# Kernel tuning notes

Hardware: AMD Instinct MI355X
Metric: run time of the kernel (lower is better)

## Reference

```python
import jax, jax.numpy as jnp
import numpy as np

H = 16; W = 16; C_IN = 32; RNN_IN = 64; HID = 128; OUT = 512; B = 512


def _upsample_bilinear_ac(x, oh, ow):
    """Bilinear upsample with align_corners=True (matches nn.UpsamplingBilinear2d). x: (B,C,h,w)."""
    h, w = x.shape[2], x.shape[3]
    ys = (jnp.arange(oh, dtype=jnp.float32) * (h - 1) / (oh - 1))
    y0 = jnp.floor(ys).astype(jnp.int32)
    y1 = jnp.minimum(y0 + 1, h - 1)
    wy = (ys - y0.astype(jnp.float32))[None, None, :, None]
    xs = (jnp.arange(ow, dtype=jnp.float32) * (w - 1) / (ow - 1))
    x0 = jnp.floor(xs).astype(jnp.int32)
    x1 = jnp.minimum(x0 + 1, w - 1)
    wx = (xs - x0.astype(jnp.float32))[None, None, None, :]
    rows = x[:, :, y0, :] * (1.0 - wy) + x[:, :, y1, :] * wy  # (B,C,oh,w)
    out = rows[:, :, :, x0] * (1.0 - wx) + rows[:, :, :, x1] * wx  # (B,C,oh,ow)
    return out


def setup_inputs() -> dict:
    key = jax.random.key(0)
    ks = jax.random.split(key, 8)
    def winit(k, shape, fan_in):
        return jax.random.normal(k, shape, jnp.float32) / np.float32(np.sqrt(fan_in))
    return {
        "x": jax.random.normal(ks[0], (B, C_IN, H, W), jnp.float32),
        "h0": jax.random.normal(ks[1], (B, HID), jnp.float32),
        "W_in": winit(ks[2], (RNN_IN, C_IN), C_IN),
        "b_in": jnp.zeros((RNN_IN,), jnp.float32),
        "W_ih": winit(ks[3], (HID, RNN_IN), RNN_IN),
        "b_ih": jnp.zeros((HID,), jnp.float32),
        "W_hh": winit(ks[4], (HID, HID), HID),
        "b_hh": jnp.zeros((HID,), jnp.float32),
        "W_out": winit(ks[5], (OUT, HID), HID),
        "b_out": jnp.zeros((OUT,), jnp.float32),
    }


def reference(x, h0, W_in, b_in, W_ih, b_ih, W_hh, b_hh, W_out, b_out):
    b = x.shape[0]
    # (B,C,H,W) -> (B,L,C), L = H*W raster order
    x_seq = x.transpose(0, 2, 3, 1).reshape(b, H * W, C_IN)
    proj = x_seq @ W_in.T + b_in                      # (B,L,RNN_IN)
    pre = proj @ W_ih.T + b_ih                        # (B,L,HID), input part of RNNCell precomputed

    def step(h, p_t):
        h_new = jnp.tanh(p_t + h @ W_hh.T + b_hh)
        return h_new, h_new

    _, hs = jax.lax.scan(step, h0, pre.transpose(1, 0, 2))  # (L,B,HID)
    hs_map = hs.reshape(H, W, b, HID).transpose(2, 3, 0, 1)  # (B,HID,H,W)
    up = _upsample_bilinear_ac(hs_map, 2 * H, 2 * W)         # (B,HID,32,32)
    act = up * jnp.clip(up + 3.0, 0.0, 6.0) * (1.0 / 6.0)    # hardswish
    pooled = act.mean(axis=(2, 3))                           # (B,HID)
    return pooled @ W_out.T + b_out
```

## Files before the change

### kernel.cpp

```cpp
#include <hip/hip_runtime.h>

#define L 256
#define BATCH 512
#define CIN 32
#define HIDN 128
#define OUTN 512

typedef _Float16 f16x8 __attribute__((ext_vector_type(8)));
typedef float f32x4 __attribute__((ext_vector_type(4)));

#define MFMA16(a, b, c) __builtin_amdgcn_mfma_f32_16x16x32_f16(a, b, c, 0, 0, 0)

static __device__ __forceinline__ unsigned short f16b(_Float16 h) {
    unsigned short u; __builtin_memcpy(&u, &h, 2); return u;
}


__global__ __launch_bounds__(512, 1) void rnn_kernel(
    const float* __restrict__ x, const float* __restrict__ h0,
    const float* __restrict__ W_in, const float* __restrict__ b_in,
    const float* __restrict__ W_ih, const float* __restrict__ b_ih,
    const float* __restrict__ W_hh, const float* __restrict__ b_hh,
    unsigned short* __restrict__ hs)
{
    const int tid = threadIdx.x;
    const int bb = blockIdx.x;
    const int lane = tid & 63;
    const int w = tid >> 6;
    const int n = lane & 15;
    const int q = lane >> 4;

    __shared__ unsigned short hbuf[2][16][HIDN];
    __shared__ unsigned short xcl[2][16][64][8];
    __shared__ float wih_s[128][65];
    __shared__ float win_s[64][32];
    __shared__ float bin_s[64];

    float4 xr[4];
    auto issue_chunk = [&](int ci) {
#pragma unroll
        for (int r = 0; r < 4; ++r) {
            int i = tid + r * 512;
            int nn = i >> 7, cc = (i >> 2) & 31, tq = i & 3;
            xr[r] = *(const float4*)(x + (((size_t)bb * 16 + nn) * CIN + cc) * L + ci * 16 + tq * 4);
        }
    };
    auto write_chunk = [&](int buf) {
#pragma unroll
        for (int r = 0; r < 4; ++r) {
            int i = tid + r * 512;
            int nn = i >> 7, cc = (i >> 2) & 31, tq = i & 3;
            int gr = ((cc >> 3) * 16 + (nn ^ ((cc >> 3) << 2))) ^ tq;
            float vv[4] = {xr[r].x, xr[r].y, xr[r].z, xr[r].w};
#pragma unroll
            for (int k = 0; k < 4; ++k)
                xcl[buf][tq * 4 + k][gr][cc & 7] = f16b((_Float16)vv[k]);
        }
    };

    issue_chunk(0);

    for (int i = tid; i < 128 * 64; i += 512) wih_s[i >> 6][i & 63] = W_ih[i];
    for (int i = tid; i < 64 * 32; i += 512) ((float*)win_s)[i] = W_in[i];
    if (tid < 64) bin_s[tid] = b_in[tid];

    if (tid < 256) {
        const int ni = tid >> 4, gi = tid & 15;
        const float4* src = (const float4*)(h0 + ((size_t)bb * 16 + ni) * HIDN + gi * 8);
        float4 a = src[0], b4 = src[1];
        float vv[8] = {a.x, a.y, a.z, a.w, b4.x, b4.y, b4.z, b4.w};
        unsigned short o[8];
#pragma unroll
        for (int i = 0; i < 8; ++i) o[i] = f16b((_Float16)vv[i]);
        *(uint4*)&hbuf[0][ni][(gi ^ (ni & 7)) * 8] = *(uint4*)o;
    }
    __syncthreads();

    const int jr = w * 16 + n;
    f16x8 Ah[4], Al[4];
    const float* wrow = W_hh + jr * HIDN;
#pragma unroll
    for (int kc = 0; kc < 4; ++kc) {
        float4 v0 = *(const float4*)(wrow + kc * 32 + q * 8);
        float4 v1 = *(const float4*)(wrow + kc * 32 + q * 8 + 4);
        float vv[8] = {v0.x, v0.y, v0.z, v0.w, v1.x, v1.y, v1.z, v1.w};
        f16x8 H, Lo;
#pragma unroll
        for (int i = 0; i < 8; ++i) {
            _Float16 hi = (_Float16)vv[i];
            H[i] = hi;
            Lo[i] = (_Float16)(vv[i] - (float)hi);
        }
        Ah[kc] = H; Al[kc] = Lo;
    }
    float acc8[8];
#pragma unroll
    for (int i = 0; i < 8; ++i) acc8[i] = 0.f;
    for (int m = 0; m < 64; ++m) {
        float wv = wih_s[jr][m];
        const float* wc = &win_s[m][q * 8];
#pragma unroll
        for (int i = 0; i < 8; ++i) acc8[i] += wv * wc[i];
    }
    f16x8 Axh, Axl;
#pragma unroll
    for (int i = 0; i < 8; ++i) {
        _Float16 hi = (_Float16)acc8[i];
        Axh[i] = hi;
        Axl[i] = (_Float16)(acc8[i] - (float)hi);
    }
    const int jb0 = w * 16 + q * 4;
    float bs4[4];
#pragma unroll
    for (int r = 0; r < 4; ++r) bs4[r] = b_ih[jb0 + r] + b_hh[jb0 + r];
    for (int m = 0; m < 64; ++m) {
        float bm = bin_s[m];
#pragma unroll
        for (int r = 0; r < 4; ++r) bs4[r] += wih_s[jb0 + r][m] * bm;
    }
    f32x4 bp = (f32x4){bs4[0], bs4[1], bs4[2], bs4[3]};
    const f32x4 zero4 = (f32x4){0.f, 0.f, 0.f, 0.f};

    write_chunk(0);
    issue_chunk(1);
    __syncthreads();

    unsigned short* hsp = hs + ((size_t)bb * 16 + n) * HIDN + w * 16 + q * 4;
    const int G = (w * 2 + (q >> 1)) ^ (n & 7);
    const int sw = n & 7;
    const int grs = q * 16 + (n ^ (q << 2));

    f16x8 xb0, xb1;
    xb0 = *(const f16x8*)&xcl[0][0][grs][0];

#define STEP(T, IN, OUT, OFF, XCUR, XNEXT)                                     \
    {                                                                          \
        f16x8 Bh0 = *(const f16x8*)&hbuf[IN][n][((0 + q) ^ sw) * 8];           \
        f16x8 Bh1 = *(const f16x8*)&hbuf[IN][n][((4 + q) ^ sw) * 8];           \
        f16x8 Bh2 = *(const f16x8*)&hbuf[IN][n][((8 + q) ^ sw) * 8];           \
        f16x8 Bh3 = *(const f16x8*)&hbuf[IN][n][((12 + q) ^ sw) * 8];          \
        f32x4 c0 = MFMA16(Axh, XCUR, bp);            \
        f32x4 c2 = MFMA16(Axl, XCUR, zero4);                                   \
        c0 = MFMA16(Ah[0], Bh0, c0);                                           \
        c2 = MFMA16(Al[0], Bh0, c2);                                           \
        f32x4 c1 = MFMA16(Ah[1], Bh1, zero4);                                  \
        f32x4 c3 = MFMA16(Al[1], Bh1, zero4);                                  \
        c0 = MFMA16(Ah[2], Bh2, c0);                                           \
        c2 = MFMA16(Al[2], Bh2, c2);                                           \
        c1 = MFMA16(Ah[3], Bh3, c1);                                           \
        c3 = MFMA16(Al[3], Bh3, c3);                                           \
        if (((T) & 15) == 14 && (T) < L - 16) {                                \
            write_chunk((((T) >> 4) & 1) ^ 1);                                 \
            if ((T) < L - 32) issue_chunk(((T) >> 4) + 2);                     \
        }                                                                      \
        f32x4 acc = (c0 + c1) + (c2 + c3);                                     \
        unsigned short o[4];                                                   \
        for (int r = 0; r < 4; ++r) {                                          \
            float e = __expf(2.f * acc[r]);                                    \
            float hv = 1.f - 2.f * __builtin_amdgcn_rcpf(e + 1.f);             \
            o[r] = f16b((_Float16)hv);                                         \
        }                                                                      \
        uint2 pk; __builtin_memcpy(&pk, o, 8);                                 \
        *(uint2*)&hbuf[OUT][n][G * 8 + (q & 1) * 4] = pk;                      \
        *(uint2*)(hsp + (OFF)) = pk;                                           \
        XNEXT = *(const f16x8*)&xcl[(((T) + 1) >> 4) & 1][((T) + 1) & 15]      \
                                  [grs ^ ((((T) + 1) & 15) >> 2)][0];          \
        asm volatile("" ::: "memory");                                         \
        __builtin_amdgcn_s_waitcnt(0xC17F);   \
        __builtin_amdgcn_s_barrier();         \
        asm volatile("" ::: "memory");                                         \
    }

    for (int t = 0; t < L; t += 2) {
        STEP(t,     0, 1, 0,             xb0, xb1);
        STEP(t + 1, 1, 0, BATCH * HIDN,  xb1, xb0);
        hsp += 2 * (BATCH * HIDN);
    }
#undef STEP
}

__global__ __launch_bounds__(256) void pool_out_kernel(
    const unsigned short* __restrict__ hs, const float* __restrict__ W_out,
    const float* __restrict__ b_out, float* __restrict__ out)
{
    const int b = blockIdx.x, tid = threadIdx.x;
    __shared__ unsigned short m[L][HIDN];
    __shared__ float ps[2][HIDN];
    __shared__ float pooled_s[HIDN];

#pragma unroll
    for (int it = 0; it < 16; ++it) {
        int i = tid + it * 256;
        int t = i >> 4, g = i & 15;
        *(uint4*)&m[t][g * 8] =
            *(const uint4*)(hs + (size_t)t * (BATCH * HIDN) + b * HIDN + g * 8);
    }
    __syncthreads();

    const int jo = tid & 127, sub = tid >> 7;
    float acc = 0.f;
    for (int oy = sub * 16; oy < sub * 16 + 16; ++oy) {
        float ysf = oy * (15.f / 31.f);
        int y0 = (int)ysf; float wy = ysf - (float)y0; int y1 = min(y0 + 1, 15);
        float rb[16];
#pragma unroll
        for (int sx = 0; sx < 16; ++sx) {
            float v0 = (float)*(const _Float16*)&m[y0 * 16 + sx][jo];
            float v1 = (float)*(const _Float16*)&m[y1 * 16 + sx][jo];
            rb[sx] = v0 + wy * (v1 - v0);
        }
#pragma unroll
        for (int ox = 0; ox < 32; ++ox) {
            float xsf = ox * (15.f / 31.f);
            int x0 = (int)xsf; float wx = xsf - (float)x0; int x1 = min(x0 + 1, 15);
            float v = rb[x0] + wx * (rb[x1] - rb[x0]);
            float t6 = fminf(fmaxf(v + 3.f, 0.f), 6.f);
            acc += v * t6;
        }
    }
    ps[sub][jo] = acc;
    __syncthreads();
    if (tid < 128) pooled_s[tid] = (ps[0][tid] + ps[1][tid]) * (1.f / 6144.f);
    __syncthreads();

    for (int o = tid; o < OUTN; o += 256) {
        float a = b_out[o];
#pragma unroll 8
        for (int k = 0; k < HIDN; k += 4) {
            float4 wv = *(const float4*)(W_out + o * HIDN + k);
            float4 pv = *(const float4*)&pooled_s[k];
            a += wv.x * pv.x + wv.y * pv.y + wv.z * pv.z + wv.w * pv.w;
        }
        out[b * OUTN + o] = a;
    }
}

extern "C" void kernel_launch(void* const* d_in, const int* in_sizes, int n_in,
                              void* d_out, int out_size, void* d_ws, size_t ws_size,
                              hipStream_t stream)
{
    const float* x     = (const float*)d_in[0];
    const float* h0    = (const float*)d_in[1];
    const float* W_in  = (const float*)d_in[2];
    const float* b_in  = (const float*)d_in[3];
    const float* W_ih  = (const float*)d_in[4];
    const float* b_ih  = (const float*)d_in[5];
    const float* W_hh  = (const float*)d_in[6];
    const float* b_hh  = (const float*)d_in[7];
    const float* W_out = (const float*)d_in[8];
    const float* b_out = (const float*)d_in[9];
    float* out = (float*)d_out;

    unsigned short* hsb = (unsigned short*)d_ws;

    rnn_kernel<<<32, 512, 0, stream>>>(x, h0, W_in, b_in, W_ih, b_ih,
                                       W_hh, b_hh, hsb);
    pool_out_kernel<<<512, 256, 0, stream>>>(hsb, W_out, b_out, out);
}
```

Before: 208.4 us.

## Store hidden states batch-major and split pooling from output GEMM

The RNN kernel now writes hidden states in batch-major layout (b, t, hid) instead of time-major, so each pooling block reads one contiguous region. Pooling is split across two blocks per batch row (64 channels each), giving 1024 blocks and less shared memory per block, and writes pooled values to a workspace buffer. The output projection moves to a separate kernel. In exchange the RNN's per-step stores become strided across batch rows, and the extra launch plus pooled round-trip through global memory add overhead.

```diff
diff --git a/kernel.cpp b/kernel.cpp
--- a/kernel.cpp
+++ b/kernel.cpp
@@ -125,7 +125,7 @@
     issue_chunk(1);
     __syncthreads();
 
-    unsigned short* hsp = hs + ((size_t)bb * 16 + n) * HIDN + w * 16 + q * 4;
+    unsigned short* hsp = hs + ((size_t)bb * 16 + n) * (L * HIDN) + w * 16 + q * 4;
     const int G = (w * 2 + (q >> 1)) ^ (n & 7);
     const int sw = n & 7;
     const int grs = q * 16 + (n ^ (q << 2));
@@ -172,34 +172,33 @@
     }
 
     for (int t = 0; t < L; t += 2) {
-        STEP(t,     0, 1, 0,             xb0, xb1);
-        STEP(t + 1, 1, 0, BATCH * HIDN,  xb1, xb0);
-        hsp += 2 * (BATCH * HIDN);
+        STEP(t,     0, 1, 0,     xb0, xb1);
+        STEP(t + 1, 1, 0, HIDN,  xb1, xb0);
+        hsp += 2 * HIDN;
     }
 #undef STEP
 }
 
-__global__ __launch_bounds__(256) void pool_out_kernel(
-    const unsigned short* __restrict__ hs, const float* __restrict__ W_out,
-    const float* __restrict__ b_out, float* __restrict__ out)
-{
-    const int b = blockIdx.x, tid = threadIdx.x;
-    __shared__ unsigned short m[L][HIDN];
-    __shared__ float ps[2][HIDN];
-    __shared__ float pooled_s[HIDN];
-
-#pragma unroll
-    for (int it = 0; it < 16; ++it) {
+__global__ __launch_bounds__(256) void pool_kernel(
+    const unsigned short* __restrict__ hs, float* __restrict__ pooled)
+{
+    const int b = blockIdx.x >> 1, jh = blockIdx.x & 1;
+    const int tid = threadIdx.x;
+    __shared__ unsigned short m[L][72];
+    __shared__ float ps[4][64];
+
+    const unsigned short* src = hs + (size_t)b * (L * HIDN) + jh * 64;
+#pragma unroll
+    for (int it = 0; it < 8; ++it) {
         int i = tid + it * 256;
-        int t = i >> 4, g = i & 15;
-        *(uint4*)&m[t][g * 8] =
-            *(const uint4*)(hs + (size_t)t * (BATCH * HIDN) + b * HIDN + g * 8);
-    }
-    __syncthreads();
-
-    const int jo = tid & 127, sub = tid >> 7;
+        int t = i >> 3, joc = i & 7;
+        *(uint4*)&m[t][joc * 8] = *(const uint4*)(src + t * HIDN + joc * 8);
+    }
+    __syncthreads();
+
+    const int jo = tid & 63, oq = tid >> 6;
     float acc = 0.f;
-    for (int oy = sub * 16; oy < sub * 16 + 16; ++oy) {
+    for (int oy = oq * 8; oy < oq * 8 + 8; ++oy) {
         float ysf = oy * (15.f / 31.f);
         int y0 = (int)ysf; float wy = ysf - (float)y0; int y1 = min(y0 + 1, 15);
         float rb[16];
@@ -218,9 +217,20 @@
             acc += v * t6;
         }
     }
-    ps[sub][jo] = acc;
-    __syncthreads();
-    if (tid < 128) pooled_s[tid] = (ps[0][tid] + ps[1][tid]) * (1.f / 6144.f);
+    ps[oq][jo] = acc;
+    __syncthreads();
+    if (tid < 64)
+        pooled[b * HIDN + jh * 64 + tid] =
+            ((ps[0][tid] + ps[1][tid]) + (ps[2][tid] + ps[3][tid])) * (1.f / 6144.f);
+}
+
+__global__ __launch_bounds__(256) void out_gemm_kernel(
+    const float* __restrict__ pooled, const float* __restrict__ W_out,
+    const float* __restrict__ b_out, float* __restrict__ out)
+{
+    const int b = blockIdx.x, tid = threadIdx.x;
+    __shared__ float pooled_s[HIDN];
+    if (tid < HIDN) pooled_s[tid] = pooled[b * HIDN + tid];
     __syncthreads();
 
     for (int o = tid; o < OUTN; o += 256) {
@@ -251,9 +261,12 @@
     const float* b_out = (const float*)d_in[9];
     float* out = (float*)d_out;
 
-    unsigned short* hsb = (unsigned short*)d_ws;
+    char* wsb = (char*)d_ws;
+    unsigned short* hsb = (unsigned short*)wsb;
+    float* pooled       = (float*)(wsb + 33554432);
 
     rnn_kernel<<<32, 512, 0, stream>>>(x, h0, W_in, b_in, W_ih, b_ih,
                                        W_hh, b_hh, hsb);
-    pool_out_kernel<<<512, 256, 0, stream>>>(hsb, W_out, b_out, out);
-}
+    pool_kernel<<<1024, 256, 0, stream>>>(hsb, pooled);
+    out_gemm_kernel<<<512, 256, 0, stream>>>(pooled, W_out, b_out, out);
+}
```

Measured after the change: 217.0 us. 1.04x slower.
